# Optimization experiments

Hardware: AMD Instinct MI355X
Metric: run time of the kernel (lower is better)

## Reference

```python
import jax, jax.numpy as jnp
import numpy as np

IMG = 416                      # image_shape
DIST = 1075.0                  # isocenter_distance
N_ANG = 320                    # 360 / rotation_resolution(=1.125 deg)
N_DET = IMG                    # detector bins
N_SAMP = IMG                   # integration samples per ray
SCALE = 512.0 / 416.0 * 0.03   # self.scale


def _ray_coords():
    """Pixel-space sample coordinates for every (angle, detector, sample).
    Returns cols, rows of shape [N_ANG, N_DET, N_SAMP] and the step length dt."""
    thetas = (jnp.arange(N_ANG, dtype=jnp.float32) * np.float32(2.0 * np.pi / N_ANG))
    half_diag = (IMG / 2.0) * np.sqrt(2.0)
    gamma_max = np.float32(np.arcsin(half_diag / DIST))  # half fan angle covering image
    gammas = jnp.linspace(-gamma_max, gamma_max, N_DET, dtype=jnp.float32)
    ray_len = np.float32(IMG * np.sqrt(2.0))             # chord length through image
    ts = jnp.linspace(np.float32(DIST - ray_len / 2.0),
                      np.float32(DIST + ray_len / 2.0), N_SAMP, dtype=jnp.float32)
    dt = float(ray_len / (N_SAMP - 1))

    th = thetas[:, None, None]        # [A,1,1]
    gm = gammas[None, :, None]        # [1,D,1]
    t = ts[None, None, :]             # [1,1,S]
    # source position on circle of radius DIST, ray direction toward detector
    sx = np.float32(DIST) * jnp.cos(th)
    sy = np.float32(DIST) * jnp.sin(th)
    x = sx - t * jnp.cos(th + gm)     # [A,D,S] world coords (isocenter at origin)
    y = sy - t * jnp.sin(th + gm)
    ctr = np.float32((IMG - 1) / 2.0)
    return x + ctr, y + ctr, dt       # pixel (col, row) coordinates


def _bilinear(img, cols, rows):
    """Zero-padded bilinear sampling of img[H,W] at float (row,col) coords."""
    c0 = jnp.floor(cols)
    r0 = jnp.floor(rows)
    wc = cols - c0
    wr = rows - r0
    c0i = c0.astype(jnp.int32)
    r0i = r0.astype(jnp.int32)

    def g(ri, ci):
        inb = (ri >= 0) & (ri < IMG) & (ci >= 0) & (ci < IMG)
        v = img[jnp.clip(ri, 0, IMG - 1), jnp.clip(ci, 0, IMG - 1)]
        return jnp.where(inb, v, jnp.float32(0.0))

    return (g(r0i, c0i) * (1 - wr) * (1 - wc)
            + g(r0i, c0i + 1) * (1 - wr) * wc
            + g(r0i + 1, c0i) * wr * (1 - wc)
            + g(r0i + 1, c0i + 1) * wr * wc)


def fan_beam_fp(vol):
    """vol: [B,H,W] -> sinogram [B, N_ANG, N_DET] via ray integration."""
    cols, rows, dt = _ray_coords()
    proj_one = lambda img: _bilinear(img, cols, rows).sum(axis=-1) * jnp.float32(dt)
    return jax.vmap(proj_one)(vol)


def setup_inputs() -> dict:
    key = jax.random.key(0)
    k1, k2 = jax.random.split(key)
    inp = jax.random.normal(k1, (1, 1, IMG, IMG), dtype=jnp.float32)
    tgt = jax.random.normal(k2, (1, 1, IMG, IMG), dtype=jnp.float32)
    return {"input": inp, "target": tgt}


def reference(input, target):
    input_proj = fan_beam_fp(input[:, 0])   # squeeze(1)
    target_proj = fan_beam_fp(target[:, 0])
    return jnp.mean((input_proj - target_proj) ** 2) * jnp.float32(SCALE)
```

## Files before the change

kernel.cpp:

```cpp
#include <hip/hip_runtime.h>
#include <math.h>

#define IMG 416
#define N_ANG 320
#define N_DET 416
#define N_SAMP 416

#define GSTRIDE 464
#define GROWS   432
#define GBYTES  ((size_t)GROWS * GSTRIDE)
#define GWORDS  (GROWS * GSTRIDE / 4)

#define SPLANE  (N_ANG * N_DET)
#define SBYTES  ((size_t)4 * SPLANE * sizeof(float))
#define WSNEED  (GBYTES + SBYTES)

#define LROWS   228
#define LWPR    59
#define LSTRIDE (LWPR * 4)

typedef float vfloat2 __attribute__((ext_vector_type(2)));

__global__ __launch_bounds__(256) void pack_kernel(const float* __restrict__ a,
                                                   const float* __restrict__ b,
                                                   unsigned int* __restrict__ G,
                                                   float* __restrict__ out) {
    int i = blockIdx.x * 256 + threadIdx.x;
    if (i == 0) out[0] = 0.0f;
    if (i >= GWORDS) return;
    int pr = i / (GSTRIDE / 4);
    int wc = i - pr * (GSTRIDE / 4);
    int r  = pr - 8;
    int c0 = wc * 4 - 8;
    float v[4];
    #pragma unroll
    for (int j = 0; j < 4; ++j) {
        int c = c0 + j;
        float val = 0.0f;
        if ((unsigned)r < (unsigned)IMG && (unsigned)c < (unsigned)IMG) {
            int idx = r * IMG + c;
            val = a[idx] - b[idx];
        }
        v[j] = val;
    }
    unsigned int u = __builtin_amdgcn_cvt_pk_fp8_f32(v[0], v[1], 0u, false);
    u = __builtin_amdgcn_cvt_pk_fp8_f32(v[2], v[3], u, true);
    G[i] = u;
}

__global__ void zero_out_kernel(float* __restrict__ out) {
    if (threadIdx.x == 0) out[0] = 0.0f;
}

__global__ __launch_bounds__(448) void proj_lds(const unsigned int* __restrict__ G,
                                                float* __restrict__ S,
                                                float theta_step, float gmax,
                                                float gstep, float t0,
                                                float dtstep) {
    __shared__ unsigned int L[LROWS * LWPR];

    const int blk = blockIdx.x;
    const int a  = blk >> 2;
    const int q  = blk & 3;
    const int qi = q >> 1, qj = q & 1;
    const int r0 = qi ? 222 : -2;
    const int c0 = qj ? 220 : -4;
    const int nrows = qi ? 198 : 228;

    {
        const int gbase = ((r0 + 8) * GSTRIDE + (c0 + 8)) >> 2;
        const int total = nrows * LWPR;
        for (int i = threadIdx.x; i < total; i += 448) {
            int rr = i / LWPR;
            int cc = i - rr * LWPR;
            L[rr * LWPR + cc] = G[gbase + rr * 116 + cc];
        }
    }
    __syncthreads();

    const int d = threadIdx.x;
    if (d < N_DET) {
        const float theta = (float)a * theta_step;
        const float gamma = fmaf((float)d, gstep, -gmax);
        float s1, c1, s2, c2;
        sincosf(theta, &s1, &c1);
        sincosf(theta + gamma, &s2, &c2);
        const float sx = fmaf(1075.0f, c1, 207.5f);
        const float sy = fmaf(1075.0f, s1, 207.5f);

        const float C0 = fmaf(-t0, c2, sx), dc = dtstep * c2;
        const float R0 = fmaf(-t0, s2, sy), dr = dtstep * s2;

        const float cl = qj ? 224.0f : -2.0f, ch = qj ? 418.0f : 224.0f;
        const float rl = qi ? 224.0f : -2.0f, rh = qi ? 418.0f : 224.0f;

        int klo = 0, khi = N_SAMP - 1;
        auto clip1 = [&](float X0, float dX, float lo, float hi) {
            if (fabsf(dX) < 1e-8f) {
                if (!(X0 >= lo && X0 < hi)) { klo = 1; khi = 0; }
            } else {
                float x1 = (X0 - hi) / dX;
                float x2 = (X0 - lo) / dX;
                x1 = fminf(fmaxf(x1, -1e6f), 1e6f);
                x2 = fminf(fmaxf(x2, -1e6f), 1e6f);
                int lo_k, hi_k;
                if (dX > 0.0f) { lo_k = (int)floorf(x1) + 1; hi_k = (int)floorf(x2); }
                else           { lo_k = (int)ceilf(x2);      hi_k = (int)ceilf(x1) - 1; }
                klo = max(klo, lo_k);
                khi = min(khi, hi_k);
            }
        };
        clip1(C0, dc, cl, ch);
        clip1(R0, dr, rl, rh);

        float acc = 0.0f;
        if (klo <= khi) {
            float colR = fmaf(-(float)klo, dc, C0) - (float)c0;
            float rowR = fmaf(-(float)klo, dr, R0) - (float)r0;
            #pragma unroll 4
            for (int k = klo; k <= khi; ++k) {
                const int ci = (int)colR;
                const int ri = (int)rowR;
                const float wc = colR - (float)ci;
                const float wr = rowR - (float)ri;
                const int bb = ri * LSTRIDE + ci;
                const int wi = bb >> 2;
                const unsigned int sh = (unsigned)(bb & 3) * 8u;
                const unsigned int w0 = L[wi];
                const unsigned int w1 = L[wi + 1];
                const unsigned int w2 = L[wi + LWPR];
                const unsigned int w3 = L[wi + LWPR + 1];
                const unsigned int top16 = __builtin_amdgcn_alignbit(w1, w0, sh);
                const unsigned int bot16 = __builtin_amdgcn_alignbit(w3, w2, sh);
                const vfloat2 X = __builtin_amdgcn_cvt_pk_f32_fp8(top16, false);
                const vfloat2 Y = __builtin_amdgcn_cvt_pk_f32_fp8(bot16, false);
                const float top = fmaf(wc, X[1] - X[0], X[0]);
                const float bot = fmaf(wc, Y[1] - Y[0], Y[0]);
                acc = fmaf(wr, bot - top, acc + top);
                colR -= dc;
                rowR -= dr;
            }
        }
        S[q * SPLANE + a * N_DET + d] = acc;
    }
}

__global__ __launch_bounds__(256) void reduce_kernel(const float* __restrict__ S,
                                                     float* __restrict__ out,
                                                     float coef) {
    const int i = blockIdx.x * 256 + threadIdx.x;
    float v = 0.0f;
    if (i < SPLANE)
        v = (S[i] + S[SPLANE + i]) + (S[2 * SPLANE + i] + S[3 * SPLANE + i]);
    float sq = v * v;
    #pragma unroll
    for (int m = 32; m > 0; m >>= 1) sq += __shfl_down(sq, m, 64);
    __shared__ float w[4];
    const int lane = threadIdx.x & 63;
    if (lane == 0) w[threadIdx.x >> 6] = sq;
    __syncthreads();
    if (threadIdx.x == 0)
        atomicAdd(out, (w[0] + w[1] + w[2] + w[3]) * coef);
}

__global__ __launch_bounds__(256) void proj_fused(const float* __restrict__ imgA,
                                                  const float* __restrict__ imgB,
                                                  float* __restrict__ out,
                                                  float theta_step, float gmax,
                                                  float gstep, float t0,
                                                  float dtstep, float coef) {
    const int idx = blockIdx.x * 256 + threadIdx.x;
    const int a  = idx / N_DET;
    const int dd = idx - a * N_DET;
    const float theta = (float)a * theta_step;
    const float gamma = fmaf((float)dd, gstep, -gmax);
    float s1, c1, s2, c2;
    sincosf(theta, &s1, &c1);
    sincosf(theta + gamma, &s2, &c2);
    const float sx = 1075.0f * c1 + 207.5f;
    const float sy = 1075.0f * s1 + 207.5f;
    float acc = 0.0f;
    #pragma unroll 4
    for (int s = 0; s < N_SAMP; ++s) {
        const float t   = fmaf((float)s, dtstep, t0);
        const float col = fmaf(-t, c2, sx);
        const float row = fmaf(-t, s2, sy);
        const float c0 = floorf(col);
        const float r0 = floorf(row);
        const float wc = col - c0;
        const float wr = row - r0;
        const int ci = (int)c0;
        const int ri = (int)r0;
        auto Gv = [&](int r, int c) -> float {
            if ((unsigned)r < (unsigned)IMG && (unsigned)c < (unsigned)IMG)
                return imgA[r * IMG + c] - imgB[r * IMG + c];
            return 0.0f;
        };
        const float v00 = Gv(ri, ci);
        const float v01 = Gv(ri, ci + 1);
        const float v10 = Gv(ri + 1, ci);
        const float v11 = Gv(ri + 1, ci + 1);
        const float top = fmaf(wc, v01 - v00, v00);
        const float bot = fmaf(wc, v11 - v10, v10);
        acc += fmaf(wr, bot - top, top);
    }
    float sq = acc * acc;
    #pragma unroll
    for (int o = 32; o > 0; o >>= 1) sq += __shfl_down(sq, o, 64);
    __shared__ float wsum[4];
    const int lane = threadIdx.x & 63;
    if (lane == 0) wsum[threadIdx.x >> 6] = sq;
    __syncthreads();
    if (threadIdx.x == 0)
        atomicAdd(out, (wsum[0] + wsum[1] + wsum[2] + wsum[3]) * coef);
}

extern "C" void kernel_launch(void* const* d_in, const int* in_sizes, int n_in,
                              void* d_out, int out_size, void* d_ws, size_t ws_size,
                              hipStream_t stream) {
    const float* in = (const float*)d_in[0];
    const float* tg = (const float*)d_in[1];
    float* out = (float*)d_out;

    const double half_diag = (IMG / 2.0) * sqrt(2.0);
    const double ray_len   = IMG * sqrt(2.0);
    const float  gmax      = (float)asin(half_diag / 1075.0);
    const float  gstep     = (float)(2.0 * (double)gmax / (N_DET - 1));
    const float  t0        = (float)(1075.0 - ray_len / 2.0);
    const float  dtstep    = (float)(ray_len / (N_SAMP - 1));
    const float  theta_step = (float)(2.0 * M_PI / N_ANG);
    const double dt        = ray_len / (N_SAMP - 1);
    const double SCALE     = 512.0 / 416.0 * 0.03;
    const float  coef      = (float)(dt * dt * SCALE / ((double)N_ANG * N_DET));

    if (ws_size >= WSNEED) {
        unsigned int* G = (unsigned int*)d_ws;
        float* S = (float*)((char*)d_ws + GBYTES);
        pack_kernel<<<(GWORDS + 255) / 256, 256, 0, stream>>>(in, tg, G, out);
        proj_lds<<<N_ANG * 4, 448, 0, stream>>>(G, S, theta_step, gmax, gstep,
                                                t0, dtstep);
        reduce_kernel<<<SPLANE / 256, 256, 0, stream>>>(S, out, coef);
    } else {
        zero_out_kernel<<<1, 64, 0, stream>>>(out);
        proj_fused<<<(N_ANG * N_DET) / 256, 256, 0, stream>>>(
            in, tg, out, theta_step, gmax, gstep, t0, dtstep, coef);
    }
}
```

Before: 110.1 us.

## Store overlapping fp8 pixel pairs and split each angle into eight tiles

The packed difference image now holds overlapping adjacent-pixel fp8 pairs, one 16-bit slot per column. The inner loop therefore does two 16-bit LDS loads per sample instead of four word loads and two alignbit shifts. Each angle is split into 2x4 tiles rather than 2x2, giving more blocks and a smaller LDS footprint per block. Partial sums go to eight planes when the workspace is large enough, otherwise to one plane via atomics. The cost is roughly double the packed image size, more redundant sincos and clipping work per ray, and a larger reduction.

```diff
diff --git a/kernel.cpp b/kernel.cpp
--- a/kernel.cpp
+++ b/kernel.cpp
@@ -6,152 +6,155 @@
 #define N_DET 416
 #define N_SAMP 416
 
-#define GSTRIDE 464
-#define GROWS   432
-#define GBYTES  ((size_t)GROWS * GSTRIDE)
-#define GWORDS  (GROWS * GSTRIDE / 4)
-
-#define SPLANE  (N_ANG * N_DET)
-#define SBYTES  ((size_t)4 * SPLANE * sizeof(float))
-#define WSNEED  (GBYTES + SBYTES)
-
-#define LROWS   228
-#define LWPR    59
-#define LSTRIDE (LWPR * 4)
+#define HSTR   216
+#define HROWS  432
+#define HWORDS (HROWS * HSTR)
+#define HBYTES ((size_t)HWORDS * 4)
+
+#define SPLANE (N_ANG * N_DET)
+#define WS_A   (HBYTES + (size_t)8 * SPLANE * 4)
+#define WS_B   (HBYTES + (size_t)SPLANE * 4)
+
+#define LWPR  55
+#define LROWS 228
+#define LDSW  (LROWS * LWPR)
 
 typedef float vfloat2 __attribute__((ext_vector_type(2)));
 
 __global__ __launch_bounds__(256) void pack_kernel(const float* __restrict__ a,
                                                    const float* __restrict__ b,
-                                                   unsigned int* __restrict__ G,
+                                                   unsigned int* __restrict__ H,
+                                                   float* __restrict__ S,
                                                    float* __restrict__ out) {
     int i = blockIdx.x * 256 + threadIdx.x;
     if (i == 0) out[0] = 0.0f;
-    if (i >= GWORDS) return;
-    int pr = i / (GSTRIDE / 4);
-    int wc = i - pr * (GSTRIDE / 4);
-    int r  = pr - 8;
-    int c0 = wc * 4 - 8;
-    float v[4];
-    #pragma unroll
-    for (int j = 0; j < 4; ++j) {
-        int c = c0 + j;
-        float val = 0.0f;
-        if ((unsigned)r < (unsigned)IMG && (unsigned)c < (unsigned)IMG) {
-            int idx = r * IMG + c;
-            val = a[idx] - b[idx];
-        }
-        v[j] = val;
-    }
-    unsigned int u = __builtin_amdgcn_cvt_pk_fp8_f32(v[0], v[1], 0u, false);
-    u = __builtin_amdgcn_cvt_pk_fp8_f32(v[2], v[3], u, true);
-    G[i] = u;
+    if (i < HWORDS) {
+        int pr  = i / HSTR;
+        int pc2 = i - pr * HSTR;
+        int r = pr - 8;
+        int c = pc2 * 2 - 8;
+        auto dv = [&](int cc) -> float {
+            bool in = ((unsigned)r < (unsigned)IMG) & ((unsigned)cc < (unsigned)IMG);
+            int idx = in ? r * IMG + cc : 0;
+            float v = a[idx] - b[idx];
+            return in ? v : 0.0f;
+        };
+        float v0 = dv(c), v1 = dv(c + 1), v2 = dv(c + 2);
+        unsigned int u = __builtin_amdgcn_cvt_pk_fp8_f32(v0, v1, 0u, false);
+        u = __builtin_amdgcn_cvt_pk_fp8_f32(v1, v2, u, true);
+        H[i] = u;
+    } else {
+        int j = i - HWORDS;
+        if (j < SPLANE) S[j] = 0.0f;
+    }
 }
 
 __global__ void zero_out_kernel(float* __restrict__ out) {
     if (threadIdx.x == 0) out[0] = 0.0f;
 }
 
-__global__ __launch_bounds__(448) void proj_lds(const unsigned int* __restrict__ G,
+__global__ __launch_bounds__(448) void proj_lds(const unsigned int* __restrict__ H,
                                                 float* __restrict__ S,
                                                 float theta_step, float gmax,
                                                 float gstep, float t0,
-                                                float dtstep) {
-    __shared__ unsigned int L[LROWS * LWPR];
+                                                float dtstep, int use8) {
+    __shared__ unsigned int L[LDSW];
 
     const int blk = blockIdx.x;
-    const int a  = blk >> 2;
-    const int q  = blk & 3;
-    const int qi = q >> 1, qj = q & 1;
-    const int r0 = qi ? 222 : -2;
-    const int c0 = qj ? 220 : -4;
-    const int nrows = qi ? 198 : 228;
+    const int a   = blk >> 3;
+    const int t   = blk & 7;
+    const int tr  = t >> 2, tc = t & 3;
+
+    const int cl_i = -2 + 105 * tc;
+    const int r0 = tr ? 222 : -2;
+    const int nrows = tr ? 198 : 228;
+    const int c0 = (cl_i - 2) & ~1;
+    const int hc0 = (c0 + 8) >> 1;
 
     {
-        const int gbase = ((r0 + 8) * GSTRIDE + (c0 + 8)) >> 2;
+        const int gbase = (r0 + 8) * HSTR + hc0;
         const int total = nrows * LWPR;
         for (int i = threadIdx.x; i < total; i += 448) {
             int rr = i / LWPR;
             int cc = i - rr * LWPR;
-            L[rr * LWPR + cc] = G[gbase + rr * 116 + cc];
+            L[rr * LWPR + cc] = H[gbase + rr * HSTR + cc];
         }
     }
     __syncthreads();
 
     const int d = threadIdx.x;
-    if (d < N_DET) {
-        const float theta = (float)a * theta_step;
-        const float gamma = fmaf((float)d, gstep, -gmax);
-        float s1, c1, s2, c2;
-        sincosf(theta, &s1, &c1);
-        sincosf(theta + gamma, &s2, &c2);
-        const float sx = fmaf(1075.0f, c1, 207.5f);
-        const float sy = fmaf(1075.0f, s1, 207.5f);
-
-        const float C0 = fmaf(-t0, c2, sx), dc = dtstep * c2;
-        const float R0 = fmaf(-t0, s2, sy), dr = dtstep * s2;
-
-        const float cl = qj ? 224.0f : -2.0f, ch = qj ? 418.0f : 224.0f;
-        const float rl = qi ? 224.0f : -2.0f, rh = qi ? 418.0f : 224.0f;
-
-        int klo = 0, khi = N_SAMP - 1;
-        auto clip1 = [&](float X0, float dX, float lo, float hi) {
-            if (fabsf(dX) < 1e-8f) {
-                if (!(X0 >= lo && X0 < hi)) { klo = 1; khi = 0; }
-            } else {
-                float x1 = (X0 - hi) / dX;
-                float x2 = (X0 - lo) / dX;
-                x1 = fminf(fmaxf(x1, -1e6f), 1e6f);
-                x2 = fminf(fmaxf(x2, -1e6f), 1e6f);
-                int lo_k, hi_k;
-                if (dX > 0.0f) { lo_k = (int)floorf(x1) + 1; hi_k = (int)floorf(x2); }
-                else           { lo_k = (int)ceilf(x2);      hi_k = (int)ceilf(x1) - 1; }
-                klo = max(klo, lo_k);
-                khi = min(khi, hi_k);
-            }
-        };
-        clip1(C0, dc, cl, ch);
-        clip1(R0, dr, rl, rh);
-
-        float acc = 0.0f;
-        if (klo <= khi) {
-            float colR = fmaf(-(float)klo, dc, C0) - (float)c0;
-            float rowR = fmaf(-(float)klo, dr, R0) - (float)r0;
-            #pragma unroll 4
-            for (int k = klo; k <= khi; ++k) {
-                const int ci = (int)colR;
-                const int ri = (int)rowR;
-                const float wc = colR - (float)ci;
-                const float wr = rowR - (float)ri;
-                const int bb = ri * LSTRIDE + ci;
-                const int wi = bb >> 2;
-                const unsigned int sh = (unsigned)(bb & 3) * 8u;
-                const unsigned int w0 = L[wi];
-                const unsigned int w1 = L[wi + 1];
-                const unsigned int w2 = L[wi + LWPR];
-                const unsigned int w3 = L[wi + LWPR + 1];
-                const unsigned int top16 = __builtin_amdgcn_alignbit(w1, w0, sh);
-                const unsigned int bot16 = __builtin_amdgcn_alignbit(w3, w2, sh);
-                const vfloat2 X = __builtin_amdgcn_cvt_pk_f32_fp8(top16, false);
-                const vfloat2 Y = __builtin_amdgcn_cvt_pk_f32_fp8(bot16, false);
-                const float top = fmaf(wc, X[1] - X[0], X[0]);
-                const float bot = fmaf(wc, Y[1] - Y[0], Y[0]);
-                acc = fmaf(wr, bot - top, acc + top);
-                colR -= dc;
-                rowR -= dr;
-            }
+    if (d >= N_DET) return;
+
+    const float theta = (float)a * theta_step;
+    const float gamma = fmaf((float)d, gstep, -gmax);
+    float s1, c1, s2, c2;
+    sincosf(theta, &s1, &c1);
+    sincosf(theta + gamma, &s2, &c2);
+    const float sx = fmaf(1075.0f, c1, 207.5f);
+    const float sy = fmaf(1075.0f, s1, 207.5f);
+
+    const float C0 = fmaf(-t0, c2, sx), dc = dtstep * c2;
+    const float R0 = fmaf(-t0, s2, sy), dr = dtstep * s2;
+
+    const float cl = (float)cl_i, ch = cl + 105.0f;
+    const float rl = tr ? 224.0f : -2.0f, rh = tr ? 418.0f : 224.0f;
+
+    int klo = 0, khi = N_SAMP - 1;
+    auto clip1 = [&](float X0, float dX, float lo, float hi) {
+        if (fabsf(dX) < 1e-8f) {
+            if (!(X0 >= lo && X0 < hi)) { klo = 1; khi = 0; }
+        } else {
+            float x1 = (X0 - hi) / dX;
+            float x2 = (X0 - lo) / dX;
+            x1 = fminf(fmaxf(x1, -1e6f), 1e6f);
+            x2 = fminf(fmaxf(x2, -1e6f), 1e6f);
+            int lo_k, hi_k;
+            if (dX > 0.0f) { lo_k = (int)floorf(x1) + 1; hi_k = (int)floorf(x2); }
+            else           { lo_k = (int)ceilf(x2);      hi_k = (int)ceilf(x1) - 1; }
+            klo = max(klo, lo_k);
+            khi = min(khi, hi_k);
         }
-        S[q * SPLANE + a * N_DET + d] = acc;
+    };
+    clip1(C0, dc, cl, ch);
+    clip1(R0, dr, rl, rh);
+
+    float acc = 0.0f;
+    if (klo <= khi) {
+        float colR = fmaf(-(float)klo, dc, C0) - (float)c0;
+        float rowR = fmaf(-(float)klo, dr, R0) - (float)r0;
+        const unsigned short* LH = (const unsigned short*)L;
+        #pragma unroll 4
+        for (int k = klo; k <= khi; ++k) {
+            const int ci = (int)colR;
+            const int ri = (int)rowR;
+            const float wcf = colR - (float)ci;
+            const float wrf = rowR - (float)ri;
+            const int e = ri * (2 * LWPR) + ci;
+            const unsigned int tp = LH[e];
+            const unsigned int bt = LH[e + 2 * LWPR];
+            const vfloat2 X = __builtin_amdgcn_cvt_pk_f32_fp8(tp, false);
+            const vfloat2 Y = __builtin_amdgcn_cvt_pk_f32_fp8(bt, false);
+            const float top = fmaf(wcf, X[1] - X[0], X[0]);
+            const float bot = fmaf(wcf, Y[1] - Y[0], Y[0]);
+            acc = fmaf(wrf, bot - top, acc + top);
+            colR -= dc;
+            rowR -= dr;
+        }
+    }
+    if (use8) {
+        S[t * SPLANE + a * N_DET + d] = acc;
+    } else if (acc != 0.0f) {
+        atomicAdd(&S[a * N_DET + d], acc);
     }
 }
 
 __global__ __launch_bounds__(256) void reduce_kernel(const float* __restrict__ S,
                                                      float* __restrict__ out,
-                                                     float coef) {
+                                                     float coef, int np) {
     const int i = blockIdx.x * 256 + threadIdx.x;
     float v = 0.0f;
     if (i < SPLANE)
-        v = (S[i] + S[SPLANE + i]) + (S[2 * SPLANE + i] + S[3 * SPLANE + i]);
+        for (int p = 0; p < np; ++p) v += S[p * SPLANE + i];
     float sq = v * v;
     #pragma unroll
     for (int m = 32; m > 0; m >>= 1) sq += __shfl_down(sq, m, 64);
@@ -233,13 +236,16 @@
     const double SCALE     = 512.0 / 416.0 * 0.03;
     const float  coef      = (float)(dt * dt * SCALE / ((double)N_ANG * N_DET));
 
-    if (ws_size >= WSNEED) {
-        unsigned int* G = (unsigned int*)d_ws;
-        float* S = (float*)((char*)d_ws + GBYTES);
-        pack_kernel<<<(GWORDS + 255) / 256, 256, 0, stream>>>(in, tg, G, out);
-        proj_lds<<<N_ANG * 4, 448, 0, stream>>>(G, S, theta_step, gmax, gstep,
-                                                t0, dtstep);
-        reduce_kernel<<<SPLANE / 256, 256, 0, stream>>>(S, out, coef);
+    if (ws_size >= WS_B) {
+        const int use8 = (ws_size >= WS_A) ? 1 : 0;
+        unsigned int* H = (unsigned int*)d_ws;
+        float* S = (float*)((char*)d_ws + HBYTES);
+        const int packN = HWORDS + SPLANE;
+        pack_kernel<<<(packN + 255) / 256, 256, 0, stream>>>(in, tg, H, S, out);
+        proj_lds<<<N_ANG * 8, 448, 0, stream>>>(H, S, theta_step, gmax, gstep,
+                                                t0, dtstep, use8);
+        reduce_kernel<<<SPLANE / 256, 256, 0, stream>>>(S, out, coef,
+                                                        use8 ? 8 : 1);
     } else {
         zero_out_kernel<<<1, 64, 0, stream>>>(out);
         proj_fused<<<(N_ANG * N_DET) / 256, 256, 0, stream>>>(
```

Result: slower. 117.3 us (+6.6%).
